# Kernel optimization log

Measured on AMD Instinct MI355X. Metric: run time of the kernel, lower is better.

Reference implementation:

```python
import jax, jax.numpy as jnp
import numpy as np

N_NODES = 50000


def _gcn_conv(x, src, dst, W, b, num_nodes):
    """PyG GCNConv: out = D^{-1/2}(A+I)D^{-1/2} (x @ W) + b, self-loops added."""
    h = x @ W  # [N, out]
    # degrees over edges incl. self-loops (src/dst already include self-loops)
    ones = jnp.ones(src.shape[0], dtype=h.dtype)
    deg = jax.ops.segment_sum(ones, dst, num_segments=num_nodes)
    dinv = jnp.where(deg > 0, jax.lax.rsqrt(deg), 0.0)
    norm = dinv[src] * dinv[dst]  # [E]
    msgs = h[src] * norm[:, None]  # [E, out] gather (memory-bound)
    out = jax.ops.segment_sum(msgs, dst, num_segments=num_nodes)
    return out + b


def setup_inputs() -> dict:
    key = jax.random.key(0)
    ks = jax.random.split(key, 8)
    in_c, h2, h1, out_c = 256, 256, 128, 128
    x = jax.random.normal(ks[0], (N_NODES, in_c), dtype=jnp.float32)
    edge_index = jax.random.randint(ks[1], (2, 800000), 0, N_NODES, dtype=jnp.int64)
    def glorot(k, fi, fo):
        s = float(np.sqrt(6.0 / (fi + fo)))
        return jax.random.uniform(k, (fi, fo), jnp.float32, -s, s)
    return {
        "x": x,
        "edge_index": edge_index,
        "W1": glorot(ks[2], in_c, h2), "b1": jnp.zeros((h2,), jnp.float32),
        "W2": glorot(ks[3], h2, h1), "b2": jnp.zeros((h1,), jnp.float32),
        "W3": glorot(ks[4], h1, out_c), "b3": jnp.zeros((out_c,), jnp.float32),
    }


def reference(x, edge_index, W1, b1, W2, b2, W3, b3):
    n = x.shape[0]
    loops = jnp.arange(n, dtype=edge_index.dtype)
    src = jnp.concatenate([edge_index[0], loops])
    dst = jnp.concatenate([edge_index[1], loops])
    # dropout is a no-op in eval mode (training=False)
    h1 = jax.nn.relu(_gcn_conv(x, src, dst, W1, b1, n))
    h2 = jax.nn.relu(_gcn_conv(h1, src, dst, W2, b2, n))
    h3 = jax.nn.relu(_gcn_conv(h2, src, dst, W3, b3, n))
    return jnp.concatenate([h1, h2, h3], axis=1)
```

## Files before the change

kernel.cpp:

```cpp
#include <hip/hip_runtime.h>

typedef __attribute__((ext_vector_type(8))) short bfrag8;
typedef __attribute__((ext_vector_type(4))) float f32x4v;

__device__ inline short f2bf(float f) {
    unsigned u = __builtin_bit_cast(unsigned, f);
    u = (u + 0x7FFFu + ((u >> 16) & 1u)) >> 16;
    return (short)u;
}
__device__ inline float bf2f(short s) {
    unsigned u = ((unsigned)(unsigned short)s) << 16;
    return __builtin_bit_cast(float, u);
}
__device__ inline int pack2(short lo, short hi) {
    return (int)(((unsigned)(unsigned short)lo) | (((unsigned)(unsigned short)hi) << 16));
}


__global__ void deg_count_kernel(const int* __restrict__ dst, int E, int* __restrict__ deg) {
    int e = blockIdx.x * blockDim.x + threadIdx.x;
    if (e < E) atomicAdd(&deg[dst[e]], 1);
}

__global__ void block_sum_kernel(const int* __restrict__ deg, int n, int* __restrict__ bsums) {
    int i = blockIdx.x * 256 + threadIdx.x;
    int v = (i < n) ? deg[i] : 0;
#pragma unroll
    for (int off = 32; off > 0; off >>= 1) v += __shfl_down(v, off);
    __shared__ int wsum[4];
    int lane = threadIdx.x & 63, w = threadIdx.x >> 6;
    if (lane == 0) wsum[w] = v;
    __syncthreads();
    if (threadIdx.x == 0) bsums[blockIdx.x] = wsum[0] + wsum[1] + wsum[2] + wsum[3];
}

__global__ void scan_bsums_kernel(int* __restrict__ bsums, int B, int* __restrict__ offs, int n) {
    __shared__ int s[256];
    int tid = threadIdx.x;
    int v = (tid < B) ? bsums[tid] : 0;
    s[tid] = v;
    __syncthreads();
    for (int off = 1; off < 256; off <<= 1) {
        int t = (tid >= off) ? s[tid - off] : 0;
        __syncthreads();
        s[tid] += t;
        __syncthreads();
    }
    if (tid < B) bsums[tid] = (tid == 0) ? 0 : s[tid - 1];
    if (tid == 0) offs[n] = s[255];
}

__global__ void scan_final_kernel(const int* __restrict__ deg, int n,
                                  const int* __restrict__ bsums,
                                  int* __restrict__ offs, int* __restrict__ cursor,
                                  float* __restrict__ dinv) {
    __shared__ int s[256];
    int tid = threadIdx.x;
    int i = blockIdx.x * 256 + tid;
    int v = (i < n) ? deg[i] : 0;
    s[tid] = v;
    __syncthreads();
    for (int off = 1; off < 256; off <<= 1) {
        int t = (tid >= off) ? s[tid - off] : 0;
        __syncthreads();
        s[tid] += t;
        __syncthreads();
    }
    if (i < n) {
        int excl = s[tid] - v + bsums[blockIdx.x];
        offs[i] = excl;
        cursor[i] = excl;
        dinv[i] = rsqrtf((float)(v + 1));
    }
}

__global__ void csr_fill_kernel(const int* __restrict__ src, const int* __restrict__ dst, int E,
                                int* __restrict__ cursor, int* __restrict__ csr) {
    int e = blockIdx.x * blockDim.x + threadIdx.x;
    if (e < E) {
        int d = dst[e];
        int p = atomicAdd(&cursor[d], 1);
        csr[p] = src[e];
    }
}


__global__ void prep_w_kernel(const float* __restrict__ W1, short* __restrict__ Wt1,
                              const float* __restrict__ W2, short* __restrict__ Wt2,
                              const float* __restrict__ W3, short* __restrict__ Wt3) {
    int i = blockIdx.x * blockDim.x + threadIdx.x;
    if (i < 65536) {
        int k = i >> 8, n = i & 255;
        Wt1[n * 256 + k] = f2bf(W1[i]);
    } else if (i < 65536 + 32768) {
        int j = i - 65536;
        int k = j >> 7, n = j & 127;
        Wt2[n * 256 + k] = f2bf(W2[j]);
    } else {
        int j = i - 65536 - 32768;
        int k = j >> 7, n = j & 127;
        Wt3[n * 128 + k] = f2bf(W3[j]);
    }
}


__global__ void x2b_kernel(const float* __restrict__ x, short* __restrict__ xb, int total8) {
    int i = blockIdx.x * blockDim.x + threadIdx.x;
    if (i < total8) {
        const float4* p = (const float4*)(x + (size_t)i * 8);
        float4 v0 = p[0], v1 = p[1];
        int4 w = make_int4(pack2(f2bf(v0.x), f2bf(v0.y)), pack2(f2bf(v0.z), f2bf(v0.w)),
                           pack2(f2bf(v1.x), f2bf(v1.y)), pack2(f2bf(v1.z), f2bf(v1.w)));
        *(int4*)(xb + (size_t)i * 8) = w;
    }
}


template<int K>
__global__ __launch_bounds__(256, 2) void gemm_skinny_kernel(
        const short* __restrict__ A,
        const short* __restrict__ Bt,
        const float* __restrict__ dinv,
        short* __restrict__ Tout, int ldt) {
    constexpr int BSTR = K + 8;
    __shared__ short Bs[64 * BSTR];

    const int tid = threadIdx.x;
    const int lane = tid & 63;
    const int wid = tid >> 6;
    const int l15 = lane & 15;
    const int quad = lane >> 4;
    const int q8 = quad * 8;
    const int bn = blockIdx.y * 64;
    const int row0 = blockIdx.x * 256 + wid * 64;

    {
        constexpr int TOT16 = 64 * K / 8;
#pragma unroll
        for (int i = tid; i < TOT16; i += 256) {
            int r = i / (K / 8);
            int c = (i % (K / 8)) * 8;
            *(int4*)&Bs[r * BSTR + c] = *(const int4*)&Bt[(size_t)(bn + r) * K + c];
        }
    }
    __syncthreads();

    f32x4v acc[4][4];
#pragma unroll
    for (int i = 0; i < 4; ++i)
#pragma unroll
        for (int j = 0; j < 4; ++j) acc[i][j] = (f32x4v){0.f, 0.f, 0.f, 0.f};

    const short* aBase = A + (size_t)(row0 + l15) * K + q8;

#pragma unroll
    for (int ks = 0; ks < K / 32; ++ks) {
        bfrag8 af[4], bf[4];
#pragma unroll
        for (int mt = 0; mt < 4; ++mt)
            af[mt] = *(const bfrag8*)(aBase + (size_t)mt * 16 * K + ks * 32);
#pragma unroll
        for (int nt = 0; nt < 4; ++nt)
            bf[nt] = *(const bfrag8*)&Bs[(nt * 16 + l15) * BSTR + ks * 32 + q8];
#pragma unroll
        for (int mt = 0; mt < 4; ++mt)
#pragma unroll
            for (int nt = 0; nt < 4; ++nt)
                acc[mt][nt] = __builtin_amdgcn_mfma_f32_16x16x32_bf16(af[mt], bf[nt], acc[mt][nt], 0, 0, 0);
    }

#pragma unroll
    for (int mt = 0; mt < 4; ++mt) {
#pragma unroll
        for (int r = 0; r < 4; ++r) {
            int grow = row0 + mt * 16 + quad * 4 + r;
            float di = dinv[grow];
            short* outp = Tout + (size_t)grow * ldt + bn + l15;
#pragma unroll
            for (int nt = 0; nt < 4; ++nt)
                outp[nt * 16] = f2bf(acc[mt][nt][r] * di);
        }
    }
}


template<bool WB>
__global__ __launch_bounds__(256) void agg256_kernel(
        const short* __restrict__ hn, const float* __restrict__ dinv,
        const int* __restrict__ offs, const int* __restrict__ csr,
        const float* __restrict__ bias, float* __restrict__ out,
        short* __restrict__ hb, int coloff, int n) {
    int node = blockIdx.x * 4 + (threadIdx.x >> 6);
    if (node >= n) return;
    int lane = threadIdx.x & 63;
    const short* base = hn + lane * 4;

    float acc[4] = {0.f, 0.f, 0.f, 0.f};
    int beg = offs[node], end = offs[node + 1];
    int e = beg;
    for (; e + 8 <= end; e += 8) {
        short4 r[8];
#pragma unroll
        for (int j = 0; j < 8; ++j)
            r[j] = *(const short4*)(base + (size_t)csr[e + j] * 256);
#pragma unroll
        for (int j = 0; j < 8; ++j) {
            acc[0] += bf2f(r[j].x); acc[1] += bf2f(r[j].y);
            acc[2] += bf2f(r[j].z); acc[3] += bf2f(r[j].w);
        }
    }
    for (; e < end; ++e) {
        short4 a = *(const short4*)(base + (size_t)csr[e] * 256);
        acc[0] += bf2f(a.x); acc[1] += bf2f(a.y); acc[2] += bf2f(a.z); acc[3] += bf2f(a.w);
    }
    {
        short4 a = *(const short4*)(base + (size_t)node * 256);
        acc[0] += bf2f(a.x); acc[1] += bf2f(a.y); acc[2] += bf2f(a.z); acc[3] += bf2f(a.w);
    }

    float di = dinv[node];
    float res[4];
#pragma unroll
    for (int v = 0; v < 4; ++v)
        res[v] = fmaxf(fmaf(di, acc[v], bias[lane * 4 + v]), 0.f);

    *(float4*)(out + (size_t)node * 512 + coloff + lane * 4) =
        make_float4(res[0], res[1], res[2], res[3]);
    if (WB) {
        int2 w = make_int2(pack2(f2bf(res[0]), f2bf(res[1])), pack2(f2bf(res[2]), f2bf(res[3])));
        *(int2*)(hb + (size_t)node * 256 + lane * 4) = w;
    }
}


template<bool WB>
__global__ __launch_bounds__(256) void agg128_kernel(
        const short* __restrict__ hn, const float* __restrict__ dinv,
        const int* __restrict__ offs, const int* __restrict__ csr,
        const float* __restrict__ bias, float* __restrict__ out,
        short* __restrict__ hb, int coloff, int n) {
    int node = blockIdx.x * 4 + (threadIdx.x >> 6);
    if (node >= n) return;
    int lane = threadIdx.x & 63;
    int hl = lane & 31;
    int half = lane >> 5;
    const short* base = hn + hl * 4;

    float acc[4] = {0.f, 0.f, 0.f, 0.f};
    int beg = offs[node], end = offs[node + 1];
    int cnt = end - beg;
    int pairs = cnt >> 1;

    int j = 0;
    for (; j + 4 <= pairs; j += 4) {
        short4 r[4];
#pragma unroll
        for (int u = 0; u < 4; ++u) {
            int s = csr[beg + 2 * (j + u) + half];
            r[u] = *(const short4*)(base + (size_t)s * 128);
        }
#pragma unroll
        for (int u = 0; u < 4; ++u) {
            acc[0] += bf2f(r[u].x); acc[1] += bf2f(r[u].y);
            acc[2] += bf2f(r[u].z); acc[3] += bf2f(r[u].w);
        }
    }
    for (; j < pairs; ++j) {
        int s = csr[beg + 2 * j + half];
        short4 r = *(const short4*)(base + (size_t)s * 128);
        acc[0] += bf2f(r.x); acc[1] += bf2f(r.y); acc[2] += bf2f(r.z); acc[3] += bf2f(r.w);
    }
    int extra;
    if (cnt & 1) extra = (half == 0) ? csr[beg + 2 * pairs] : node;
    else         extra = (half == 0) ? node : -1;
    if (extra >= 0) {
        short4 r = *(const short4*)(base + (size_t)extra * 128);
        acc[0] += bf2f(r.x); acc[1] += bf2f(r.y); acc[2] += bf2f(r.z); acc[3] += bf2f(r.w);
    }

#pragma unroll
    for (int v = 0; v < 4; ++v) acc[v] += __shfl_xor(acc[v], 32);

    if (half == 0) {
        float di = dinv[node];
        float res[4];
#pragma unroll
        for (int v = 0; v < 4; ++v)
            res[v] = fmaxf(fmaf(di, acc[v], bias[hl * 4 + v]), 0.f);
        *(float4*)(out + (size_t)node * 512 + coloff + hl * 4) =
            make_float4(res[0], res[1], res[2], res[3]);
        if (WB) {
            int2 w = make_int2(pack2(f2bf(res[0]), f2bf(res[1])), pack2(f2bf(res[2]), f2bf(res[3])));
            *(int2*)(hb + (size_t)node * 128 + hl * 4) = w;
        }
    }
}


extern "C" void kernel_launch(void* const* d_in, const int* in_sizes, int n_in,
                              void* d_out, int out_size, void* d_ws, size_t ws_size,
                              hipStream_t stream) {
    const float* x  = (const float*)d_in[0];
    const int*   ei = (const int*)d_in[1];
    const float* W1 = (const float*)d_in[2];
    const float* b1 = (const float*)d_in[3];
    const float* W2 = (const float*)d_in[4];
    const float* b2 = (const float*)d_in[5];
    const float* W3 = (const float*)d_in[6];
    const float* b3 = (const float*)d_in[7];

    const int IN_C = 256, H2 = 256, H1 = 128, OUT_C = 128;
    int n = in_sizes[0] / IN_C;
    int E = in_sizes[1] / 2;
    const int* src = ei;
    const int* dst = ei + E;

    int sb = (n + 255) / 256;
    int npad = sb * 256;

    char* ws = (char*)d_ws;
    auto carve = [&](size_t bytes) { char* p = ws; ws += (bytes + 255) & ~(size_t)255; return p; };
    int*   deg    = (int*)  carve((size_t)n * 4);
    int*   offs   = (int*)  carve(((size_t)n + 1) * 4);
    int*   cursor = (int*)  carve((size_t)n * 4);
    float* dinv   = (float*)carve((size_t)npad * 4);
    int*   csr    = (int*)  carve((size_t)E * 4);
    int*   bsums  = (int*)  carve(256 * 4);
    short* Wt1    = (short*)carve((size_t)IN_C * H2 * 2);
    short* Wt2    = (short*)carve((size_t)H2 * H1 * 2);
    short* Wt3    = (short*)carve((size_t)H1 * OUT_C * 2);
    short* t      = (short*)carve((size_t)npad * 256 * 2);
    short* inb    = (short*)carve((size_t)npad * 256 * 2);

    float* out = (float*)d_out;
    int nblk = (n + 255) / 256;

    hipMemsetAsync(deg, 0, (size_t)n * sizeof(int), stream);
    deg_count_kernel<<<(E + 255) / 256, 256, 0, stream>>>(dst, E, deg);
    block_sum_kernel<<<nblk, 256, 0, stream>>>(deg, n, bsums);
    scan_bsums_kernel<<<1, 256, 0, stream>>>(bsums, nblk, offs, n);
    scan_final_kernel<<<nblk, 256, 0, stream>>>(deg, n, bsums, offs, cursor, dinv);
    csr_fill_kernel<<<(E + 255) / 256, 256, 0, stream>>>(src, dst, E, cursor, csr);

    prep_w_kernel<<<(65536 + 32768 + 16384 + 255) / 256, 256, 0, stream>>>(W1, Wt1, W2, Wt2, W3, Wt3);

    int total8 = n * IN_C / 8;
    x2b_kernel<<<(total8 + 255) / 256, 256, 0, stream>>>(x, inb, total8);

    gemm_skinny_kernel<256><<<dim3(sb, H2 / 64), 256, 0, stream>>>(inb, Wt1, dinv, t, H2);
    agg256_kernel<true><<<(n + 3) / 4, 256, 0, stream>>>(t, dinv, offs, csr, b1, out, inb, 0, n);

    gemm_skinny_kernel<256><<<dim3(sb, H1 / 64), 256, 0, stream>>>(inb, Wt2, dinv, t, H1);
    agg128_kernel<true><<<(n + 3) / 4, 256, 0, stream>>>(t, dinv, offs, csr, b2, out, inb, H2, n);

    gemm_skinny_kernel<128><<<dim3(sb, OUT_C / 64), 256, 0, stream>>>(inb, Wt3, dinv, t, OUT_C);
    agg128_kernel<false><<<(n + 3) / 4, 256, 0, stream>>>(t, dinv, offs, csr, b3, out, nullptr, H2 + H1, n);
}
```

Measured before the change: 429.0 us.

## Slice aggregation by feature columns across XCDs and fold self-loops into CSR

The aggregation kernels are replaced by one templated kernel. It splits the feature dimension into 32-column slices, and the block index is mapped so that each XCD handles one slice, keeping that slice of the gathered feature table resident in its L2. Self-loops are now inserted into the CSR during the scan, so the separate self-loop gather goes away. Non-temporal loads and stores are used for the CSR indices and outputs. In exchange, each wave handles 8 nodes serially with 4-byte gathers and a cross-lane reduction, which lowers memory-level parallelism per request and relies on round-robin XCD block placement.

```diff
diff --git a/kernel.cpp b/kernel.cpp
--- a/kernel.cpp
+++ b/kernel.cpp
@@ -2,6 +2,7 @@
 
 typedef __attribute__((ext_vector_type(8))) short bfrag8;
 typedef __attribute__((ext_vector_type(4))) float f32x4v;
+typedef __attribute__((ext_vector_type(2))) float f32x2;
 
 __device__ inline short f2bf(float f) {
     unsigned u = __builtin_bit_cast(unsigned, f);
@@ -24,7 +25,7 @@
 
 __global__ void block_sum_kernel(const int* __restrict__ deg, int n, int* __restrict__ bsums) {
     int i = blockIdx.x * 256 + threadIdx.x;
-    int v = (i < n) ? deg[i] : 0;
+    int v = (i < n) ? deg[i] + 1 : 0;
 #pragma unroll
     for (int off = 32; off > 0; off >>= 1) v += __shfl_down(v, off);
     __shared__ int wsum[4];
@@ -53,11 +54,11 @@
 __global__ void scan_final_kernel(const int* __restrict__ deg, int n,
                                   const int* __restrict__ bsums,
                                   int* __restrict__ offs, int* __restrict__ cursor,
-                                  float* __restrict__ dinv) {
+                                  float* __restrict__ dinv, int* __restrict__ csr) {
     __shared__ int s[256];
     int tid = threadIdx.x;
     int i = blockIdx.x * 256 + tid;
-    int v = (i < n) ? deg[i] : 0;
+    int v = (i < n) ? deg[i] + 1 : 0;
     s[tid] = v;
     __syncthreads();
     for (int off = 1; off < 256; off <<= 1) {
@@ -69,8 +70,9 @@
     if (i < n) {
         int excl = s[tid] - v + bsums[blockIdx.x];
         offs[i] = excl;
-        cursor[i] = excl;
-        dinv[i] = rsqrtf((float)(v + 1));
+        csr[excl] = i;
+        cursor[i] = excl + 1;
+        dinv[i] = rsqrtf((float)v);
     }
 }
 
@@ -184,114 +186,62 @@
 }
 
 
-template<bool WB>
-__global__ __launch_bounds__(256) void agg256_kernel(
+template<int C, int NS, bool WB>
+__global__ __launch_bounds__(256) void agg_slice_kernel(
         const short* __restrict__ hn, const float* __restrict__ dinv,
         const int* __restrict__ offs, const int* __restrict__ csr,
         const float* __restrict__ bias, float* __restrict__ out,
         short* __restrict__ hb, int coloff, int n) {
-    int node = blockIdx.x * 4 + (threadIdx.x >> 6);
-    if (node >= n) return;
-    int lane = threadIdx.x & 63;
-    const short* base = hn + lane * 4;
-
-    float acc[4] = {0.f, 0.f, 0.f, 0.f};
-    int beg = offs[node], end = offs[node + 1];
-    int e = beg;
-    for (; e + 8 <= end; e += 8) {
-        short4 r[8];
-#pragma unroll
-        for (int j = 0; j < 8; ++j)
-            r[j] = *(const short4*)(base + (size_t)csr[e + j] * 256);
-#pragma unroll
-        for (int j = 0; j < 8; ++j) {
-            acc[0] += bf2f(r[j].x); acc[1] += bf2f(r[j].y);
-            acc[2] += bf2f(r[j].z); acc[3] += bf2f(r[j].w);
-        }
-    }
-    for (; e < end; ++e) {
-        short4 a = *(const short4*)(base + (size_t)csr[e] * 256);
-        acc[0] += bf2f(a.x); acc[1] += bf2f(a.y); acc[2] += bf2f(a.z); acc[3] += bf2f(a.w);
-    }
-    {
-        short4 a = *(const short4*)(base + (size_t)node * 256);
-        acc[0] += bf2f(a.x); acc[1] += bf2f(a.y); acc[2] += bf2f(a.z); acc[3] += bf2f(a.w);
-    }
-
-    float di = dinv[node];
-    float res[4];
-#pragma unroll
-    for (int v = 0; v < 4; ++v)
-        res[v] = fmaxf(fmaf(di, acc[v], bias[lane * 4 + v]), 0.f);
-
-    *(float4*)(out + (size_t)node * 512 + coloff + lane * 4) =
-        make_float4(res[0], res[1], res[2], res[3]);
-    if (WB) {
-        int2 w = make_int2(pack2(f2bf(res[0]), f2bf(res[1])), pack2(f2bf(res[2]), f2bf(res[3])));
-        *(int2*)(hb + (size_t)node * 256 + lane * 4) = w;
-    }
-}
-
-
-template<bool WB>
-__global__ __launch_bounds__(256) void agg128_kernel(
-        const short* __restrict__ hn, const float* __restrict__ dinv,
-        const int* __restrict__ offs, const int* __restrict__ csr,
-        const float* __restrict__ bias, float* __restrict__ out,
-        short* __restrict__ hb, int coloff, int n) {
-    int node = blockIdx.x * 4 + (threadIdx.x >> 6);
-    if (node >= n) return;
-    int lane = threadIdx.x & 63;
-    int hl = lane & 31;
-    int half = lane >> 5;
-    const short* base = hn + hl * 4;
-
-    float acc[4] = {0.f, 0.f, 0.f, 0.f};
-    int beg = offs[node], end = offs[node + 1];
-    int cnt = end - beg;
-    int pairs = cnt >> 1;
-
-    int j = 0;
-    for (; j + 4 <= pairs; j += 4) {
-        short4 r[4];
-#pragma unroll
-        for (int u = 0; u < 4; ++u) {
-            int s = csr[beg + 2 * (j + u) + half];
-            r[u] = *(const short4*)(base + (size_t)s * 128);
-        }
-#pragma unroll
-        for (int u = 0; u < 4; ++u) {
-            acc[0] += bf2f(r[u].x); acc[1] += bf2f(r[u].y);
-            acc[2] += bf2f(r[u].z); acc[3] += bf2f(r[u].w);
-        }
-    }
-    for (; j < pairs; ++j) {
-        int s = csr[beg + 2 * j + half];
-        short4 r = *(const short4*)(base + (size_t)s * 128);
-        acc[0] += bf2f(r.x); acc[1] += bf2f(r.y); acc[2] += bf2f(r.z); acc[3] += bf2f(r.w);
-    }
-    int extra;
-    if (cnt & 1) extra = (half == 0) ? csr[beg + 2 * pairs] : node;
-    else         extra = (half == 0) ? node : -1;
-    if (extra >= 0) {
-        short4 r = *(const short4*)(base + (size_t)extra * 128);
-        acc[0] += bf2f(r.x); acc[1] += bf2f(r.y); acc[2] += bf2f(r.z); acc[3] += bf2f(r.w);
-    }
-
-#pragma unroll
-    for (int v = 0; v < 4; ++v) acc[v] += __shfl_xor(acc[v], 32);
-
-    if (half == 0) {
-        float di = dinv[node];
-        float res[4];
-#pragma unroll
-        for (int v = 0; v < 4; ++v)
-            res[v] = fmaxf(fmaf(di, acc[v], bias[hl * 4 + v]), 0.f);
-        *(float4*)(out + (size_t)node * 512 + coloff + hl * 4) =
-            make_float4(res[0], res[1], res[2], res[3]);
-        if (WB) {
-            int2 w = make_int2(pack2(f2bf(res[0]), f2bf(res[1])), pack2(f2bf(res[2]), f2bf(res[3])));
-            *(int2*)(hb + (size_t)node * 128 + hl * 4) = w;
+    constexpr int DUP = 8 / NS;
+    const int xcd = blockIdx.x & 7;
+    const int k = blockIdx.x >> 3;
+    const int slice = xcd & (NS - 1);
+    const int chunk = k * DUP + (xcd / NS);
+    const int wid = threadIdx.x >> 6;
+    const int lane = threadIdx.x & 63;
+    const int sub = lane >> 4;
+    const int ch = lane & 15;
+    const int node0 = chunk * 32 + wid * 8;
+    if (node0 >= n) return;
+    const int nend = min(node0 + 8, n);
+    const short* base = hn + slice * 32 + ch * 2;
+
+    for (int node = node0; node < nend; ++node) {
+        int beg = offs[node], end = offs[node + 1];
+        float ax = 0.f, ay = 0.f;
+        int e = beg + sub;
+        for (; e + 4 < end; e += 8) {
+            int s0 = __builtin_nontemporal_load(csr + e);
+            int s1 = __builtin_nontemporal_load(csr + e + 4);
+            int v0 = *(const int*)(base + (size_t)s0 * C);
+            int v1 = *(const int*)(base + (size_t)s1 * C);
+            ax += __builtin_bit_cast(float, v0 << 16);
+            ay += __builtin_bit_cast(float, (int)(v0 & 0xFFFF0000));
+            ax += __builtin_bit_cast(float, v1 << 16);
+            ay += __builtin_bit_cast(float, (int)(v1 & 0xFFFF0000));
+        }
+        if (e < end) {
+            int s0 = __builtin_nontemporal_load(csr + e);
+            int v0 = *(const int*)(base + (size_t)s0 * C);
+            ax += __builtin_bit_cast(float, v0 << 16);
+            ay += __builtin_bit_cast(float, (int)(v0 & 0xFFFF0000));
+        }
+        ax += __shfl_xor(ax, 16); ax += __shfl_xor(ax, 32);
+        ay += __shfl_xor(ay, 16); ay += __shfl_xor(ay, 32);
+        if (sub == 0) {
+            float di = dinv[node];
+            float b0 = bias[slice * 32 + ch * 2];
+            float b1 = bias[slice * 32 + ch * 2 + 1];
+            float r0 = fmaxf(fmaf(di, ax, b0), 0.f);
+            float r1 = fmaxf(fmaf(di, ay, b1), 0.f);
+            f32x2 w; w.x = r0; w.y = r1;
+            __builtin_nontemporal_store(w,
+                (f32x2*)(out + (size_t)node * 512 + coloff + slice * 32 + ch * 2));
+            if (WB) {
+                int wb = pack2(f2bf(r0), f2bf(r1));
+                __builtin_nontemporal_store(wb,
+                    (int*)(hb + (size_t)node * C + slice * 32 + ch * 2));
+            }
         }
     }
 }
@@ -324,7 +274,7 @@
     int*   offs   = (int*)  carve(((size_t)n + 1) * 4);
     int*   cursor = (int*)  carve((size_t)n * 4);
     float* dinv   = (float*)carve((size_t)npad * 4);
-    int*   csr    = (int*)  carve((size_t)E * 4);
+    int*   csr    = (int*)  carve(((size_t)E + n) * 4);
     int*   bsums  = (int*)  carve(256 * 4);
     short* Wt1    = (short*)carve((size_t)IN_C * H2 * 2);
     short* Wt2    = (short*)carve((size_t)H2 * H1 * 2);
@@ -339,7 +289,7 @@
     deg_count_kernel<<<(E + 255) / 256, 256, 0, stream>>>(dst, E, deg);
     block_sum_kernel<<<nblk, 256, 0, stream>>>(deg, n, bsums);
     scan_bsums_kernel<<<1, 256, 0, stream>>>(bsums, nblk, offs, n);
-    scan_final_kernel<<<nblk, 256, 0, stream>>>(deg, n, bsums, offs, cursor, dinv);
+    scan_final_kernel<<<nblk, 256, 0, stream>>>(deg, n, bsums, offs, cursor, dinv, csr);
     csr_fill_kernel<<<(E + 255) / 256, 256, 0, stream>>>(src, dst, E, cursor, csr);
 
     prep_w_kernel<<<(65536 + 32768 + 16384 + 255) / 256, 256, 0, stream>>>(W1, Wt1, W2, Wt2, W3, Wt3);
@@ -347,12 +297,16 @@
     int total8 = n * IN_C / 8;
     x2b_kernel<<<(total8 + 255) / 256, 256, 0, stream>>>(x, inb, total8);
 
+    int nchunks = (n + 31) / 32;
+    int gx8 = 8 * nchunks;
+    int gx4 = 8 * ((nchunks + 1) / 2);
+
     gemm_skinny_kernel<256><<<dim3(sb, H2 / 64), 256, 0, stream>>>(inb, Wt1, dinv, t, H2);
-    agg256_kernel<true><<<(n + 3) / 4, 256, 0, stream>>>(t, dinv, offs, csr, b1, out, inb, 0, n);
+    agg_slice_kernel<256, 8, true><<<gx8, 256, 0, stream>>>(t, dinv, offs, csr, b1, out, inb, 0, n);
 
     gemm_skinny_kernel<256><<<dim3(sb, H1 / 64), 256, 0, stream>>>(inb, Wt2, dinv, t, H1);
-    agg128_kernel<true><<<(n + 3) / 4, 256, 0, stream>>>(t, dinv, offs, csr, b2, out, inb, H2, n);
+    agg_slice_kernel<128, 4, true><<<gx4, 256, 0, stream>>>(t, dinv, offs, csr, b2, out, inb, H2, n);
 
     gemm_skinny_kernel<128><<<dim3(sb, OUT_C / 64), 256, 0, stream>>>(inb, Wt3, dinv, t, OUT_C);
-    agg128_kernel<false><<<(n + 3) / 4, 256, 0, stream>>>(t, dinv, offs, csr, b3, out, nullptr, H2 + H1, n);
-}
+    agg_slice_kernel<128, 4, false><<<gx4, 256, 0, stream>>>(t, dinv, offs, csr, b3, out, nullptr, H2 + H1, n);
+}
```

Result: slower. 745.4 us (+73.8%).

## Pad CSR rows to multiples of 16 with dummy node and widen gather loads

Applied to the files above, without the earlier changes.

Each node's CSR row now holds the self-loop first and is padded with a dummy index n to a multiple of 16. Padded rows in the activation buffers are zeroed and dinv for those rows is set to zero, so padded entries contribute nothing. The aggregation kernels drop their tail handling and use 16-byte bf16x8 gathers, with several sub-groups of lanes working on different edges and reducing via shuffles. The cost is a larger CSR array, the writes that fill the padding, and wasted gathers on padded slots.

```diff
diff --git a/kernel.cpp b/kernel.cpp
--- a/kernel.cpp
+++ b/kernel.cpp
@@ -15,6 +15,7 @@
 __device__ inline int pack2(short lo, short hi) {
     return (int)(((unsigned)(unsigned short)lo) | (((unsigned)(unsigned short)hi) << 16));
 }
+__device__ inline int pad16i(int v) { return (v + 15) & ~15; }
 
 
 __global__ void deg_count_kernel(const int* __restrict__ dst, int E, int* __restrict__ deg) {
@@ -24,7 +25,7 @@
 
 __global__ void block_sum_kernel(const int* __restrict__ deg, int n, int* __restrict__ bsums) {
     int i = blockIdx.x * 256 + threadIdx.x;
-    int v = (i < n) ? deg[i] : 0;
+    int v = (i < n) ? pad16i(deg[i] + 1) : 0;
 #pragma unroll
     for (int off = 32; off > 0; off >>= 1) v += __shfl_down(v, off);
     __shared__ int wsum[4];
@@ -53,12 +54,13 @@
 __global__ void scan_final_kernel(const int* __restrict__ deg, int n,
                                   const int* __restrict__ bsums,
                                   int* __restrict__ offs, int* __restrict__ cursor,
-                                  float* __restrict__ dinv) {
+                                  float* __restrict__ dinv, int* __restrict__ csr) {
     __shared__ int s[256];
     int tid = threadIdx.x;
     int i = blockIdx.x * 256 + tid;
-    int v = (i < n) ? deg[i] : 0;
-    s[tid] = v;
+    int vt = (i < n) ? deg[i] + 1 : 0;
+    int pv = (i < n) ? pad16i(vt) : 0;
+    s[tid] = pv;
     __syncthreads();
     for (int off = 1; off < 256; off <<= 1) {
         int t = (tid >= off) ? s[tid - off] : 0;
@@ -67,10 +69,14 @@
         __syncthreads();
     }
     if (i < n) {
-        int excl = s[tid] - v + bsums[blockIdx.x];
+        int excl = s[tid] - pv + bsums[blockIdx.x];
         offs[i] = excl;
-        cursor[i] = excl;
-        dinv[i] = rsqrtf((float)(v + 1));
+        csr[excl] = i;
+        cursor[i] = excl + 1;
+        for (int p = excl + vt; p < excl + pv; ++p) csr[p] = n;
+        dinv[i] = rsqrtf((float)vt);
+    } else {
+        dinv[i] = 0.f;
     }
 }
 
@@ -104,7 +110,8 @@
 }
 
 
-__global__ void x2b_kernel(const float* __restrict__ x, short* __restrict__ xb, int total8) {
+__global__ void x2b_kernel(const float* __restrict__ x, short* __restrict__ xb,
+                           int total8, int totalp8) {
     int i = blockIdx.x * blockDim.x + threadIdx.x;
     if (i < total8) {
         const float4* p = (const float4*)(x + (size_t)i * 8);
@@ -112,6 +119,8 @@
         int4 w = make_int4(pack2(f2bf(v0.x), f2bf(v0.y)), pack2(f2bf(v0.z), f2bf(v0.w)),
                            pack2(f2bf(v1.x), f2bf(v1.y)), pack2(f2bf(v1.z), f2bf(v1.w)));
         *(int4*)(xb + (size_t)i * 8) = w;
+    } else if (i < totalp8) {
+        *(int4*)(xb + (size_t)i * 8) = make_int4(0, 0, 0, 0);
     }
 }
 
@@ -193,42 +202,45 @@
     int node = blockIdx.x * 4 + (threadIdx.x >> 6);
     if (node >= n) return;
     int lane = threadIdx.x & 63;
-    const short* base = hn + lane * 4;
-
-    float acc[4] = {0.f, 0.f, 0.f, 0.f};
+    int hl = lane & 31;
+    int sub = lane >> 5;
+    const short* base = hn + hl * 8;
+
+    float acc[8];
+#pragma unroll
+    for (int v = 0; v < 8; ++v) acc[v] = 0.f;
+
     int beg = offs[node], end = offs[node + 1];
-    int e = beg;
-    for (; e + 8 <= end; e += 8) {
-        short4 r[8];
+    for (int e = beg + sub; e < end; e += 16) {
+        int s[8];
+#pragma unroll
+        for (int j = 0; j < 8; ++j) s[j] = csr[e + 2 * j];
+        bfrag8 r[8];
+#pragma unroll
+        for (int j = 0; j < 8; ++j) r[j] = *(const bfrag8*)(base + (size_t)s[j] * 256);
 #pragma unroll
         for (int j = 0; j < 8; ++j)
-            r[j] = *(const short4*)(base + (size_t)csr[e + j] * 256);
-#pragma unroll
-        for (int j = 0; j < 8; ++j) {
-            acc[0] += bf2f(r[j].x); acc[1] += bf2f(r[j].y);
-            acc[2] += bf2f(r[j].z); acc[3] += bf2f(r[j].w);
+#pragma unroll
+            for (int v = 0; v < 8; ++v) acc[v] += bf2f(r[j][v]);
+    }
+
+#pragma unroll
+    for (int v = 0; v < 8; ++v) acc[v] += __shfl_xor(acc[v], 32);
+
+    if (sub == 0) {
+        float di = dinv[node];
+        float res[8];
+#pragma unroll
+        for (int v = 0; v < 8; ++v)
+            res[v] = fmaxf(fmaf(di, acc[v], bias[hl * 8 + v]), 0.f);
+        float4* op = (float4*)(out + (size_t)node * 512 + coloff + hl * 8);
+        op[0] = make_float4(res[0], res[1], res[2], res[3]);
+        op[1] = make_float4(res[4], res[5], res[6], res[7]);
+        if (WB) {
+            int4 w = make_int4(pack2(f2bf(res[0]), f2bf(res[1])), pack2(f2bf(res[2]), f2bf(res[3])),
+                               pack2(f2bf(res[4]), f2bf(res[5])), pack2(f2bf(res[6]), f2bf(res[7])));
+            *(int4*)(hb + (size_t)node * 256 + hl * 8) = w;
         }
-    }
-    for (; e < end; ++e) {
-        short4 a = *(const short4*)(base + (size_t)csr[e] * 256);
-        acc[0] += bf2f(a.x); acc[1] += bf2f(a.y); acc[2] += bf2f(a.z); acc[3] += bf2f(a.w);
-    }
-    {
-        short4 a = *(const short4*)(base + (size_t)node * 256);
-        acc[0] += bf2f(a.x); acc[1] += bf2f(a.y); acc[2] += bf2f(a.z); acc[3] += bf2f(a.w);
-    }
-
-    float di = dinv[node];
-    float res[4];
-#pragma unroll
-    for (int v = 0; v < 4; ++v)
-        res[v] = fmaxf(fmaf(di, acc[v], bias[lane * 4 + v]), 0.f);
-
-    *(float4*)(out + (size_t)node * 512 + coloff + lane * 4) =
-        make_float4(res[0], res[1], res[2], res[3]);
-    if (WB) {
-        int2 w = make_int2(pack2(f2bf(res[0]), f2bf(res[1])), pack2(f2bf(res[2]), f2bf(res[3])));
-        *(int2*)(hb + (size_t)node * 256 + lane * 4) = w;
     }
 }
 
@@ -242,56 +254,60 @@
     int node = blockIdx.x * 4 + (threadIdx.x >> 6);
     if (node >= n) return;
     int lane = threadIdx.x & 63;
-    int hl = lane & 31;
-    int half = lane >> 5;
-    const short* base = hn + hl * 4;
-
-    float acc[4] = {0.f, 0.f, 0.f, 0.f};
+    int ch = lane & 15;
+    int sub = lane >> 4;
+    const short* base = hn + ch * 8;
+
+    float acc[8];
+#pragma unroll
+    for (int v = 0; v < 8; ++v) acc[v] = 0.f;
+
     int beg = offs[node], end = offs[node + 1];
-    int cnt = end - beg;
-    int pairs = cnt >> 1;
-
-    int j = 0;
-    for (; j + 4 <= pairs; j += 4) {
-        short4 r[4];
-#pragma unroll
-        for (int u = 0; u < 4; ++u) {
-            int s = csr[beg + 2 * (j + u) + half];
-            r[u] = *(const short4*)(base + (size_t)s * 128);
-        }
-#pragma unroll
-        for (int u = 0; u < 4; ++u) {
-            acc[0] += bf2f(r[u].x); acc[1] += bf2f(r[u].y);
-            acc[2] += bf2f(r[u].z); acc[3] += bf2f(r[u].w);
-        }
-    }
-    for (; j < pairs; ++j) {
-        int s = csr[beg + 2 * j + half];
-        short4 r = *(const short4*)(base + (size_t)s * 128);
-        acc[0] += bf2f(r.x); acc[1] += bf2f(r.y); acc[2] += bf2f(r.z); acc[3] += bf2f(r.w);
-    }
-    int extra;
-    if (cnt & 1) extra = (half == 0) ? csr[beg + 2 * pairs] : node;
-    else         extra = (half == 0) ? node : -1;
-    if (extra >= 0) {
-        short4 r = *(const short4*)(base + (size_t)extra * 128);
-        acc[0] += bf2f(r.x); acc[1] += bf2f(r.y); acc[2] += bf2f(r.z); acc[3] += bf2f(r.w);
-    }
-
-#pragma unroll
-    for (int v = 0; v < 4; ++v) acc[v] += __shfl_xor(acc[v], 32);
-
-    if (half == 0) {
+    int e = beg + sub;
+    for (; e + 16 < end; e += 32) {
+        int s[8];
+#pragma unroll
+        for (int j = 0; j < 8; ++j) s[j] = csr[e + 4 * j];
+        bfrag8 r[8];
+#pragma unroll
+        for (int j = 0; j < 8; ++j) r[j] = *(const bfrag8*)(base + (size_t)s[j] * 128);
+#pragma unroll
+        for (int j = 0; j < 8; ++j)
+#pragma unroll
+            for (int v = 0; v < 8; ++v) acc[v] += bf2f(r[j][v]);
+    }
+    if (e < end) {
+        int s[4];
+#pragma unroll
+        for (int j = 0; j < 4; ++j) s[j] = csr[e + 4 * j];
+        bfrag8 r[4];
+#pragma unroll
+        for (int j = 0; j < 4; ++j) r[j] = *(const bfrag8*)(base + (size_t)s[j] * 128);
+#pragma unroll
+        for (int j = 0; j < 4; ++j)
+#pragma unroll
+            for (int v = 0; v < 8; ++v) acc[v] += bf2f(r[j][v]);
+    }
+
+#pragma unroll
+    for (int v = 0; v < 8; ++v) {
+        acc[v] += __shfl_xor(acc[v], 16);
+        acc[v] += __shfl_xor(acc[v], 32);
+    }
+
+    if (sub == 0) {
         float di = dinv[node];
-        float res[4];
-#pragma unroll
-        for (int v = 0; v < 4; ++v)
-            res[v] = fmaxf(fmaf(di, acc[v], bias[hl * 4 + v]), 0.f);
-        *(float4*)(out + (size_t)node * 512 + coloff + hl * 4) =
-            make_float4(res[0], res[1], res[2], res[3]);
+        float res[8];
+#pragma unroll
+        for (int v = 0; v < 8; ++v)
+            res[v] = fmaxf(fmaf(di, acc[v], bias[ch * 8 + v]), 0.f);
+        float4* op = (float4*)(out + (size_t)node * 512 + coloff + ch * 8);
+        op[0] = make_float4(res[0], res[1], res[2], res[3]);
+        op[1] = make_float4(res[4], res[5], res[6], res[7]);
         if (WB) {
-            int2 w = make_int2(pack2(f2bf(res[0]), f2bf(res[1])), pack2(f2bf(res[2]), f2bf(res[3])));
-            *(int2*)(hb + (size_t)node * 128 + hl * 4) = w;
+            int4 w = make_int4(pack2(f2bf(res[0]), f2bf(res[1])), pack2(f2bf(res[2]), f2bf(res[3])),
+                               pack2(f2bf(res[4]), f2bf(res[5])), pack2(f2bf(res[6]), f2bf(res[7])));
+            *(int4*)(hb + (size_t)node * 128 + ch * 8) = w;
         }
     }
 }
@@ -324,7 +340,7 @@
     int*   offs   = (int*)  carve(((size_t)n + 1) * 4);
     int*   cursor = (int*)  carve((size_t)n * 4);
     float* dinv   = (float*)carve((size_t)npad * 4);
-    int*   csr    = (int*)  carve((size_t)E * 4);
+    int*   csr    = (int*)  carve(((size_t)E + 16 * (size_t)n) * 4);
     int*   bsums  = (int*)  carve(256 * 4);
     short* Wt1    = (short*)carve((size_t)IN_C * H2 * 2);
     short* Wt2    = (short*)carve((size_t)H2 * H1 * 2);
@@ -339,13 +355,14 @@
     deg_count_kernel<<<(E + 255) / 256, 256, 0, stream>>>(dst, E, deg);
     block_sum_kernel<<<nblk, 256, 0, stream>>>(deg, n, bsums);
     scan_bsums_kernel<<<1, 256, 0, stream>>>(bsums, nblk, offs, n);
-    scan_final_kernel<<<nblk, 256, 0, stream>>>(deg, n, bsums, offs, cursor, dinv);
+    scan_final_kernel<<<nblk, 256, 0, stream>>>(deg, n, bsums, offs, cursor, dinv, csr);
     csr_fill_kernel<<<(E + 255) / 256, 256, 0, stream>>>(src, dst, E, cursor, csr);
 
     prep_w_kernel<<<(65536 + 32768 + 16384 + 255) / 256, 256, 0, stream>>>(W1, Wt1, W2, Wt2, W3, Wt3);
 
     int total8 = n * IN_C / 8;
-    x2b_kernel<<<(total8 + 255) / 256, 256, 0, stream>>>(x, inb, total8);
+    int totalp8 = npad * IN_C / 8;
+    x2b_kernel<<<(totalp8 + 255) / 256, 256, 0, stream>>>(x, inb, total8, totalp8);
 
     gemm_skinny_kernel<256><<<dim3(sb, H2 / 64), 256, 0, stream>>>(inb, Wt1, dinv, t, H2);
     agg256_kernel<true><<<(n + 3) / 4, 256, 0, stream>>>(t, dinv, offs, csr, b1, out, inb, 0, n);
@@ -353,6 +370,8 @@
     gemm_skinny_kernel<256><<<dim3(sb, H1 / 64), 256, 0, stream>>>(inb, Wt2, dinv, t, H1);
     agg128_kernel<true><<<(n + 3) / 4, 256, 0, stream>>>(t, dinv, offs, csr, b2, out, inb, H2, n);
 
+    hipMemsetAsync(inb + (size_t)n * 128, 0, (size_t)(npad - n) * 128 * 2, stream);
+
     gemm_skinny_kernel<128><<<dim3(sb, OUT_C / 64), 256, 0, stream>>>(inb, Wt3, dinv, t, OUT_C);
     agg128_kernel<false><<<(n + 3) / 4, 256, 0, stream>>>(t, dinv, offs, csr, b3, out, nullptr, H2 + H1, n);
 }
```

New measurement: 419.3 us. -2.3%, faster.
